# Kernel optimization log

Hardware: AMD Instinct MI355X
Metric: run time of the kernel (lower is better)

## Reference

```python
import jax, jax.numpy as jnp
import numpy as np

WS = 8                       # window size (square)
N = WS * WS                  # tokens per window
RES_H, RES_W = 32, 32        # input_resolution
DIM = 512
NUM_HEADS = 16
HEAD_DIM = DIM // NUM_HEADS
SCALE = HEAD_DIM ** -0.5
TABLE = 2 * WS - 1           # size of a_p/b_p/a_r/b_r tables
B_ = 1024                    # num_windows * batch


def _rel_coords():
    c = np.arange(WS)
    coords = np.stack(np.meshgrid(c, c, indexing='ij'))          # (2, WS, WS)
    cf = coords.reshape(2, -1)                                   # (2, N)
    rel = cf[:, :, None] - cf[:, None, :]                        # (2, N, N), values in [-(WS-1), WS-1]
    return rel[0], rel[1]                                        # radius (dh), azimuth (dw)

RADIUS_NP, AZIMUTH_NP = _rel_coords()
# torch indexes the (2*WS-1)-row tables with negative indices -> python wrap: -k maps to TABLE-k
IDX_R = jnp.asarray(RADIUS_NP % TABLE)
IDX_AZ = jnp.asarray(AZIMUTH_NP % TABLE)
RADIUS = jnp.asarray(RADIUS_NP, dtype=jnp.float32)               # (N, N)
AZIMUTH = jnp.asarray(AZIMUTH_NP, dtype=jnp.float32)             # (N, N)


def setup_inputs() -> dict:
    key = jax.random.key(0)
    ks = jax.random.split(key, 10)
    return {
        'x': jax.random.normal(ks[0], (B_, N, DIM), dtype=jnp.float32),
        'theta_max': jnp.ones((), dtype=jnp.float32) * 1.5708,   # ~pi/2 field-of-view half-angle
        'qkv_w': jax.random.normal(ks[1], (3 * DIM, DIM), dtype=jnp.float32) * 0.02,
        'qkv_b': jnp.zeros((3 * DIM,), dtype=jnp.float32),
        'proj_w': jax.random.normal(ks[2], (DIM, DIM), dtype=jnp.float32) * 0.02,
        'proj_b': jnp.zeros((DIM,), dtype=jnp.float32),
        'a_p': jax.random.normal(ks[3], (TABLE, NUM_HEADS), dtype=jnp.float32) * 0.02,
        'b_p': jax.random.normal(ks[4], (TABLE, NUM_HEADS), dtype=jnp.float32) * 0.02,
        'a_r': jax.random.normal(ks[5], (TABLE, NUM_HEADS), dtype=jnp.float32) * 0.02,
        'b_r': jax.random.normal(ks[6], (TABLE, NUM_HEADS), dtype=jnp.float32) * 0.02,
    }


def _trig_bias(table_a, table_b, idx, angle):
    # table_[ab]: (TABLE, H); idx: (N, N) int; angle: (N, N) float (possibly traced)
    a = table_a[idx]                                              # (N, N, H)
    b = table_b[idx]
    ang = angle[:, :, None]                                       # (N, N, 1)
    bias = a * jnp.cos(ang) + b * jnp.sin(ang)                    # (N, N, H)
    return jnp.transpose(bias, (2, 0, 1))                         # (H, N, N)


def reference(x, theta_max, qkv_w, qkv_b, proj_w, proj_b, a_p, b_p, a_r, b_r):
    Bw, n, c = x.shape
    qkv = x @ qkv_w.T + qkv_b                                     # (B_, N, 3*DIM)
    qkv = qkv.reshape(Bw, n, 3, NUM_HEADS, HEAD_DIM)
    qkv = jnp.transpose(qkv, (2, 0, 3, 1, 4))                     # (3, B_, H, N, hd)
    q, k, v = qkv[0] * SCALE, qkv[1], qkv[2]

    attn = jnp.einsum('bhid,bhjd->bhij', q, k)                    # (B_, H, N, N)

    az_angle = AZIMUTH * (2.0 * np.pi / RES_W)                    # (N, N)
    A_phi = _trig_bias(a_p, b_p, IDX_AZ, az_angle)                # (H, N, N)
    r_angle = RADIUS * (theta_max / RES_H)                        # (N, N), traced via theta_max
    A_theta = _trig_bias(a_r, b_r, IDX_R, r_angle)                # (H, N, N)

    attn = attn + A_phi[None] + A_theta[None]
    attn = jax.nn.softmax(attn, axis=-1)

    out = jnp.einsum('bhij,bhjd->bhid', attn, v)                  # (B_, H, N, hd)
    out = jnp.transpose(out, (0, 2, 1, 3)).reshape(Bw, n, c)      # (B_, N, DIM)
    out = out @ proj_w.T + proj_b
    return out
```

## Files before the change

kernel.cpp:

```cpp
#include <hip/hip_runtime.h>
#include <hip/hip_bf16.h>


typedef __bf16 bf16_t;
typedef bf16_t bf16x4 __attribute__((ext_vector_type(4)));
typedef bf16_t bf16x8 __attribute__((ext_vector_type(8)));
typedef float  f32x4  __attribute__((ext_vector_type(4)));

#define NWIN   1024
#define NTOK   64
#define DIM    512
#define NHEADS 16
#define HD     32
#define MTOT   (NWIN*NTOK)
#define QKVN   (3*DIM)
#define SCLG2E 0.25503494f

__device__ __forceinline__ void async_copy16(const void* g, void* lds_generic) {
    __builtin_amdgcn_global_load_lds(
        (__attribute__((address_space(1))) unsigned int*)(unsigned long long)g,
        (__attribute__((address_space(3))) unsigned int*)(unsigned int)(unsigned long long)lds_generic,
        16, 0, 0);
}

__global__ void cvt_f32_bf16(const float* __restrict__ in, bf16_t* __restrict__ out, int n8) {
    int i = blockIdx.x * blockDim.x + threadIdx.x;
    if (i >= n8) return;
    const float4* p = (const float4*)in;
    float4 a = p[2*i], b = p[2*i+1];
    bf16x8 o;
    o[0]=(bf16_t)a.x; o[1]=(bf16_t)a.y; o[2]=(bf16_t)a.z; o[3]=(bf16_t)a.w;
    o[4]=(bf16_t)b.x; o[5]=(bf16_t)b.y; o[6]=(bf16_t)b.z; o[7]=(bf16_t)b.w;
    ((bf16x8*)out)[i] = o;
}

__global__ void bias_kernel(const float* __restrict__ ap, const float* __restrict__ bp,
                            const float* __restrict__ ar, const float* __restrict__ br,
                            const float* __restrict__ theta_max, float* __restrict__ bias) {
    int idx = blockIdx.x * 256 + threadIdx.x;
    int h  = idx >> 12;
    int ij = idx & 4095;
    int i = ij >> 6, j = ij & 63;
    int ri = i >> 3, ci = i & 7, rj = j >> 3, cj = j & 7;
    int rad = ri - rj, az = ci - cj;
    int idx_r  = rad < 0 ? rad + 15 : rad;
    int idx_az = az  < 0 ? az  + 15 : az;
    float azang = (float)az * 0.19634954084936207f;
    float rang  = (float)rad * (theta_max[0] * (1.0f/32.0f));
    float v = ap[idx_az*NHEADS + h] * cosf(azang) + bp[idx_az*NHEADS + h] * sinf(azang)
            + ar[idx_r *NHEADS + h] * cosf(rang)  + br[idx_r *NHEADS + h] * sinf(rang);
    bias[idx] = v * 1.4426950408889634f;
}

template<int OUT_BF16>
__global__ __launch_bounds__(512, 2)
void gemm_bt(const bf16_t* __restrict__ A, const bf16_t* __restrict__ Bt,
             const float* __restrict__ bias, void* __restrict__ C,
             int M, int N, int K, int ntiles) {
    __shared__ bf16_t sA[3][256*64];
    __shared__ bf16_t sB[3][128*64];

    int nwg = gridDim.x;
    int bid = blockIdx.x;
    int wg = ((nwg & 7) == 0) ? ((bid & 7) * (nwg >> 3) + (bid >> 3)) : bid;
    int bm = wg / ntiles, bn = wg % ntiles;

    int tid = threadIdx.x;
    int w = tid >> 6, lane = tid & 63;
    int quad = lane >> 4, l16 = lane & 15;
    int wm = w >> 2, wn = w & 3;

    const bf16_t* Abase = A  + (size_t)(bm*256) * K;
    const bf16_t* Bbase = Bt + (size_t)(bn*128) * K;

    int T = K >> 6;

    auto STAGE = [&](int t) {
        int q = t - (t/3)*3;
        int k0 = t << 6;
        #pragma unroll
        for (int i = 0; i < 4; ++i) {
            int off = (i*512 + tid) << 4;
            int r  = off >> 7;
            int pb = (off >> 4) & 7;
            int cb = pb ^ (r & 7);
            async_copy16(Abase + (size_t)r*K + k0 + cb*8,
                         (char*)sA[q] + i*8192 + w*1024);
        }
        #pragma unroll
        for (int i = 0; i < 2; ++i) {
            int off = (i*512 + tid) << 4;
            int r  = off >> 7;
            int pb = (off >> 4) & 7;
            int cb = pb ^ (r & 7);
            async_copy16(Bbase + (size_t)r*K + k0 + cb*8,
                         (char*)sB[q] + i*8192 + w*1024);
        }
    };

    f32x4 acc[8][2] = {};

    STAGE(0);
    if (T > 1) STAGE(1);

    #pragma unroll 1
    for (int t = 0; t < T; ++t) {
        if (t < T - 1) asm volatile("s_waitcnt vmcnt(6)" ::: "memory");
        else           asm volatile("s_waitcnt vmcnt(0)" ::: "memory");
        __builtin_amdgcn_s_barrier();
        if (t + 2 < T) STAGE(t + 2);

        int q = t - (t/3)*3;
        const char* cA = (const char*)sA[q];
        const char* cB = (const char*)sB[q];
        #pragma unroll
        for (int kk = 0; kk < 64; kk += 32) {
            bf16x8 af[8], bfr[2];
            #pragma unroll
            for (int mi = 0; mi < 8; ++mi) {
                int r  = wm*128 + mi*16 + l16;
                int cb = (kk >> 3) + quad;
                int pb = cb ^ (r & 7);
                af[mi] = *(const bf16x8*)(cA + r*128 + pb*16);
            }
            #pragma unroll
            for (int ni = 0; ni < 2; ++ni) {
                int r  = wn*32 + ni*16 + l16;
                int cb = (kk >> 3) + quad;
                int pb = cb ^ (r & 7);
                bfr[ni] = *(const bf16x8*)(cB + r*128 + pb*16);
            }
            #pragma unroll
            for (int mi = 0; mi < 8; ++mi)
                #pragma unroll
                for (int ni = 0; ni < 2; ++ni)
                    acc[mi][ni] = __builtin_amdgcn_mfma_f32_16x16x32_bf16(
                        af[mi], bfr[ni], acc[mi][ni], 0, 0, 0);
        }
    }

    #pragma unroll
    for (int ni = 0; ni < 2; ++ni) {
        int col = bn*128 + wn*32 + ni*16 + l16;
        float bv = bias[col];
        #pragma unroll
        for (int mi = 0; mi < 8; ++mi) {
            int row0 = bm*256 + wm*128 + mi*16 + quad*4;
            f32x4 a = acc[mi][ni];
            #pragma unroll
            for (int reg = 0; reg < 4; ++reg) {
                float v = a[reg] + bv;
                size_t o = (size_t)(row0 + reg) * N + col;
                if (OUT_BF16) ((bf16_t*)C)[o] = (bf16_t)v;
                else          ((float*)C)[o]  = v;
            }
        }
    }
}

__global__ __launch_bounds__(256, 4)
void attn_kernel(const bf16_t* __restrict__ qkv, const float* __restrict__ bias,
                 bf16_t* __restrict__ obuf) {
    __shared__ bf16_t pbuf[4][2048];

    int b = blockIdx.x;
    int tid = threadIdx.x;
    int w = tid >> 6, lane = tid & 63, quad = lane >> 4, l16 = lane & 15;
    int qh = quad >> 1, ql = quad & 1;
    const bf16_t* base = qkv + (size_t)(b*64) * QKVN;
    f32x4 zero = {0.f, 0.f, 0.f, 0.f};
    bf16_t* pb = pbuf[w];

    #pragma unroll 1
    for (int t = 0; t < 4; ++t) {
        int h = w*4 + t;

        bf16x8 ak[4], bq[4];
        #pragma unroll
        for (int jt = 0; jt < 4; ++jt)
            ak[jt] = *(const bf16x8*)(base + (size_t)(jt*16 + l16)*QKVN + 512 + h*32 + quad*8);
        #pragma unroll
        for (int it = 0; it < 4; ++it)
            bq[it] = *(const bf16x8*)(base + (size_t)(it*16 + l16)*QKVN + h*32 + quad*8);

        bf16x8 av[2][2];
        #pragma unroll
        for (int dt = 0; dt < 2; ++dt)
            #pragma unroll
            for (int ks = 0; ks < 2; ++ks) {
                const bf16_t* vb = base + (size_t)(ks*32 + quad*8)*QKVN + 1024 + h*32 + dt*16 + l16;
                bf16x8 tmp;
                #pragma unroll
                for (int e = 0; e < 8; ++e) tmp[e] = vb[(size_t)e*QKVN];
                av[dt][ks] = tmp;
            }

        const float* bh = bias + h*4096;
        f32x4 accO[2][4];
        float s[4];
        #pragma unroll
        for (int it = 0; it < 4; ++it) { s[it] = 0.f; accO[0][it] = zero; accO[1][it] = zero; }

        #pragma unroll
        for (int ks = 0; ks < 2; ++ks) {
            f32x4 bb[2][4];
            #pragma unroll
            for (int jh = 0; jh < 2; ++jh)
                #pragma unroll
                for (int it = 0; it < 4; ++it)
                    bb[jh][it] = *(const f32x4*)(bh + (it*16 + l16)*64 + (ks*2+jh)*16 + quad*4);

            f32x4 st[2][4];
            #pragma unroll
            for (int jh = 0; jh < 2; ++jh)
                #pragma unroll
                for (int it = 0; it < 4; ++it)
                    st[jh][it] = __builtin_amdgcn_mfma_f32_16x16x32_bf16(ak[ks*2+jh], bq[it], zero, 0, 0, 0);

            #pragma unroll
            for (int it = 0; it < 4; ++it)
                #pragma unroll
                for (int jh = 0; jh < 2; ++jh) {
                    float e0 = __builtin_amdgcn_exp2f(st[jh][it][0]*SCLG2E + bb[jh][it][0]);
                    float e1 = __builtin_amdgcn_exp2f(st[jh][it][1]*SCLG2E + bb[jh][it][1]);
                    float e2 = __builtin_amdgcn_exp2f(st[jh][it][2]*SCLG2E + bb[jh][it][2]);
                    float e3 = __builtin_amdgcn_exp2f(st[jh][it][3]*SCLG2E + bb[jh][it][3]);
                    s[it] += (e0 + e1) + (e2 + e3);
                    bf16x4 pk4;
                    pk4[0] = (bf16_t)e0; pk4[1] = (bf16_t)e1;
                    pk4[2] = (bf16_t)e2; pk4[3] = (bf16_t)e3;
                    *(bf16x4*)(pb + it*512 + (2*jh + qh)*128 + l16*8 + ql*4) = pk4;
                }

            #pragma unroll
            for (int it = 0; it < 4; ++it) {
                bf16x8 bp = ((const bf16x8*)(pb + it*512))[lane];
                accO[0][it] = __builtin_amdgcn_mfma_f32_16x16x32_bf16(av[0][ks], bp, accO[0][it], 0, 0, 0);
                accO[1][it] = __builtin_amdgcn_mfma_f32_16x16x32_bf16(av[1][ks], bp, accO[1][it], 0, 0, 0);
            }
        }

        #pragma unroll
        for (int it = 0; it < 4; ++it) {
            float sv = s[it];
            sv += __shfl_xor(sv, 16);
            sv += __shfl_xor(sv, 32);
            float inv = __builtin_amdgcn_rcpf(sv);
            #pragma unroll
            for (int dt = 0; dt < 2; ++dt) {
                bf16x4 o4;
                #pragma unroll
                for (int r = 0; r < 4; ++r) o4[r] = (bf16_t)(accO[dt][it][r] * inv);
                *(bf16x4*)(obuf + (size_t)(b*64 + it*16 + l16)*DIM + h*32 + dt*16 + quad*4) = o4;
            }
        }
    }
}

extern "C" void kernel_launch(void* const* d_in, const int* in_sizes, int n_in,
                              void* d_out, int out_size, void* d_ws, size_t ws_size,
                              hipStream_t stream) {
    const float* x      = (const float*)d_in[0];
    const float* theta  = (const float*)d_in[1];
    const float* qkv_w  = (const float*)d_in[2];
    const float* qkv_b  = (const float*)d_in[3];
    const float* proj_w = (const float*)d_in[4];
    const float* proj_b = (const float*)d_in[5];
    const float* a_p    = (const float*)d_in[6];
    const float* b_p    = (const float*)d_in[7];
    const float* a_r    = (const float*)d_in[8];
    const float* b_r    = (const float*)d_in[9];
    float* out = (float*)d_out;

    char* ws = (char*)d_ws;
    bf16_t* qkvbuf = (bf16_t*)ws;
    bf16_t* xb     = (bf16_t*)(ws + 201326592);
    bf16_t* wqkv   = (bf16_t*)(ws + 201326592 + 67108864);
    bf16_t* wproj  = (bf16_t*)(ws + 201326592 + 67108864 + 1572864);
    float*  biasbf = (float*) (ws + 201326592 + 67108864 + 1572864 + 524288);
    bf16_t* obuf   = xb;

    cvt_f32_bf16<<<(MTOT*DIM/8)/256, 256, 0, stream>>>(x, xb, MTOT*DIM/8);
    cvt_f32_bf16<<<(QKVN*DIM/8)/256, 256, 0, stream>>>(qkv_w, wqkv, QKVN*DIM/8);
    cvt_f32_bf16<<<(DIM*DIM/8)/256, 256, 0, stream>>>(proj_w, wproj, DIM*DIM/8);

    bias_kernel<<<256, 256, 0, stream>>>(a_p, b_p, a_r, b_r, theta, biasbf);

    gemm_bt<1><<<(MTOT/256)*(QKVN/128), 512, 0, stream>>>(xb, wqkv, qkv_b, qkvbuf,
                                                          MTOT, QKVN, DIM, QKVN/128);
    attn_kernel<<<NWIN, 256, 0, stream>>>(qkvbuf, biasbf, obuf);

    gemm_bt<0><<<(MTOT/256)*(DIM/128), 512, 0, stream>>>(obuf, wproj, proj_b, out,
                                                         MTOT, DIM, DIM, DIM/128);
}
```

Baseline: 561.6 us.

## Rework GEMM to 256x256 tiles with half-K ping-pong LDS pipeline

The bf16 GEMM used for the QKV and output projections now computes 256x256 output tiles instead of 256x128. It double-buffers LDS in 32-wide K halves with a new XOR swizzle. Async global-to-LDS loads are interleaved with MFMA phases separated by barriers and raised wave priority, in the style of a ping-pong schedule. This is meant to raise arithmetic intensity per tile and hide load latency. In exchange it doubles the accumulator registers, halves the grid size, which lowers occupancy and tail balance, and adds many barriers.

New measurement: 679.7 us. +21.0%, slower.

```diff
diff --git a/kernel.cpp b/kernel.cpp
--- a/kernel.cpp
+++ b/kernel.cpp
@@ -15,6 +15,8 @@
 #define MTOT   (NWIN*NTOK)
 #define QKVN   (3*DIM)
 #define SCLG2E 0.25503494f
+
+#define BAR()  do { __builtin_amdgcn_s_barrier(); asm volatile("" ::: "memory"); } while (0)
 
 __device__ __forceinline__ void async_copy16(const void* g, void* lds_generic) {
     __builtin_amdgcn_global_load_lds(
@@ -57,8 +59,7 @@
 void gemm_bt(const bf16_t* __restrict__ A, const bf16_t* __restrict__ Bt,
              const float* __restrict__ bias, void* __restrict__ C,
              int M, int N, int K, int ntiles) {
-    __shared__ bf16_t sA[3][256*64];
-    __shared__ bf16_t sB[3][128*64];
+    __shared__ bf16_t lds[2][2][2][8192];
 
     int nwg = gridDim.x;
     int bid = blockIdx.x;
@@ -71,77 +72,99 @@
     int wm = w >> 2, wn = w & 3;
 
     const bf16_t* Abase = A  + (size_t)(bm*256) * K;
-    const bf16_t* Bbase = Bt + (size_t)(bn*128) * K;
+    const bf16_t* Bbase = Bt + (size_t)(bn*256) * K;
 
     int T = K >> 6;
-
-    auto STAGE = [&](int t) {
-        int q = t - (t/3)*3;
-        int k0 = t << 6;
-        #pragma unroll
-        for (int i = 0; i < 4; ++i) {
-            int off = (i*512 + tid) << 4;
-            int r  = off >> 7;
-            int pb = (off >> 4) & 7;
-            int cb = pb ^ (r & 7);
-            async_copy16(Abase + (size_t)r*K + k0 + cb*8,
-                         (char*)sA[q] + i*8192 + w*1024);
-        }
-        #pragma unroll
-        for (int i = 0; i < 2; ++i) {
-            int off = (i*512 + tid) << 4;
-            int r  = off >> 7;
-            int pb = (off >> 4) & 7;
-            int cb = pb ^ (r & 7);
-            async_copy16(Bbase + (size_t)r*K + k0 + cb*8,
-                         (char*)sB[q] + i*8192 + w*1024);
+    int niter = T >> 1;
+
+    auto STAGE = [&](const bf16_t* Mb, int mat, int t, int h) {
+        int q = t & 1;
+        int k0 = (t << 6) + (h << 5);
+        char* dst = (char*)&lds[q][mat][h][0] + w*1024;
+        #pragma unroll
+        for (int j = 0; j < 2; ++j) {
+            int slot = j*512 + tid;
+            int r  = slot >> 2;
+            int cb = (slot & 3) ^ ((r >> 1) & 3);
+            async_copy16(Mb + (size_t)r*K + k0 + cb*8, dst + j*8192);
         }
     };
 
-    f32x4 acc[8][2] = {};
-
-    STAGE(0);
-    if (T > 1) STAGE(1);
+    auto LDA = [&](int q, int h, bf16x8* af) {
+        const char* b_ = (const char*)&lds[q][0][h][0];
+        #pragma unroll
+        for (int mi = 0; mi < 8; ++mi) {
+            int r = wm*128 + mi*16 + l16;
+            af[mi] = *(const bf16x8*)(b_ + r*64 + ((quad ^ ((r >> 1) & 3)) << 4));
+        }
+    };
+    auto LDB = [&](int q, int h, int n0, bf16x8* bf2) {
+        const char* b_ = (const char*)&lds[q][1][h][0];
+        #pragma unroll
+        for (int k = 0; k < 2; ++k) {
+            int r = wn*64 + (n0 + k)*16 + l16;
+            bf2[k] = *(const bf16x8*)(b_ + r*64 + ((quad ^ ((r >> 1) & 3)) << 4));
+        }
+    };
+
+    f32x4 acc[8][4] = {};
+
+    auto MMA = [&](bf16x8* af, bf16x8* bf2, int n0) {
+        __builtin_amdgcn_s_setprio(1);
+        #pragma unroll
+        for (int mi = 0; mi < 8; ++mi)
+            #pragma unroll
+            for (int k = 0; k < 2; ++k)
+                acc[mi][n0 + k] = __builtin_amdgcn_mfma_f32_16x16x32_bf16(
+                    af[mi], bf2[k], acc[mi][n0 + k], 0, 0, 0);
+        __builtin_amdgcn_s_setprio(0);
+    };
+
+    STAGE(Abase, 0, 0, 0); STAGE(Bbase, 1, 0, 0);
+    STAGE(Abase, 0, 0, 1); STAGE(Bbase, 1, 0, 1);
+    STAGE(Abase, 0, 1, 0); STAGE(Bbase, 1, 1, 0);
+    asm volatile("s_waitcnt vmcnt(4)" ::: "memory");
+    BAR();
 
     #pragma unroll 1
-    for (int t = 0; t < T; ++t) {
-        if (t < T - 1) asm volatile("s_waitcnt vmcnt(6)" ::: "memory");
-        else           asm volatile("s_waitcnt vmcnt(0)" ::: "memory");
-        __builtin_amdgcn_s_barrier();
-        if (t + 2 < T) STAGE(t + 2);
-
-        int q = t - (t/3)*3;
-        const char* cA = (const char*)sA[q];
-        const char* cB = (const char*)sB[q];
-        #pragma unroll
-        for (int kk = 0; kk < 64; kk += 32) {
-            bf16x8 af[8], bfr[2];
-            #pragma unroll
-            for (int mi = 0; mi < 8; ++mi) {
-                int r  = wm*128 + mi*16 + l16;
-                int cb = (kk >> 3) + quad;
-                int pb = cb ^ (r & 7);
-                af[mi] = *(const bf16x8*)(cA + r*128 + pb*16);
-            }
-            #pragma unroll
-            for (int ni = 0; ni < 2; ++ni) {
-                int r  = wn*32 + ni*16 + l16;
-                int cb = (kk >> 3) + quad;
-                int pb = cb ^ (r & 7);
-                bfr[ni] = *(const bf16x8*)(cB + r*128 + pb*16);
-            }
-            #pragma unroll
-            for (int mi = 0; mi < 8; ++mi)
-                #pragma unroll
-                for (int ni = 0; ni < 2; ++ni)
-                    acc[mi][ni] = __builtin_amdgcn_mfma_f32_16x16x32_bf16(
-                        af[mi], bfr[ni], acc[mi][ni], 0, 0, 0);
-        }
+    for (int i = 0; i < niter; ++i) {
+        int t0 = 2*i, t1 = 2*i + 1;
+        bool last = (i == niter - 1);
+        bf16x8 af[8], bf2[2];
+
+        LDA(0, 0, af); LDB(0, 0, 0, bf2);
+        STAGE(Abase, 0, t1, 1);
+        BAR(); MMA(af, bf2, 0); BAR();
+        LDB(0, 0, 2, bf2);
+        STAGE(Bbase, 1, t1, 1);
+        BAR(); MMA(af, bf2, 2); BAR();
+        LDA(0, 1, af); LDB(0, 1, 0, bf2);
+        if (t0 + 2 < T) STAGE(Abase, 0, t0 + 2, 0);
+        BAR(); MMA(af, bf2, 0); BAR();
+        LDB(0, 1, 2, bf2);
+        if (t0 + 2 < T) STAGE(Bbase, 1, t0 + 2, 0);
+        if (last) asm volatile("s_waitcnt vmcnt(0)" ::: "memory");
+        else      asm volatile("s_waitcnt vmcnt(4)" ::: "memory");
+        BAR(); MMA(af, bf2, 2); BAR();
+        LDA(1, 0, af); LDB(1, 0, 0, bf2);
+        if (t0 + 2 < T) STAGE(Abase, 0, t0 + 2, 1);
+        BAR(); MMA(af, bf2, 0); BAR();
+        LDB(1, 0, 2, bf2);
+        if (t0 + 2 < T) STAGE(Bbase, 1, t0 + 2, 1);
+        BAR(); MMA(af, bf2, 2); BAR();
+        LDA(1, 1, af); LDB(1, 1, 0, bf2);
+        if (t1 + 2 < T) STAGE(Abase, 0, t1 + 2, 0);
+        BAR(); MMA(af, bf2, 0); BAR();
+        LDB(1, 1, 2, bf2);
+        if (t1 + 2 < T) STAGE(Bbase, 1, t1 + 2, 0);
+        if (last) asm volatile("s_waitcnt vmcnt(0)" ::: "memory");
+        else      asm volatile("s_waitcnt vmcnt(4)" ::: "memory");
+        BAR(); MMA(af, bf2, 2); BAR();
     }
 
     #pragma unroll
-    for (int ni = 0; ni < 2; ++ni) {
-        int col = bn*128 + wn*32 + ni*16 + l16;
+    for (int ni = 0; ni < 4; ++ni) {
+        int col = bn*256 + wn*64 + ni*16 + l16;
         float bv = bias[col];
         #pragma unroll
         for (int mi = 0; mi < 8; ++mi) {
@@ -286,10 +309,10 @@
 
     bias_kernel<<<256, 256, 0, stream>>>(a_p, b_p, a_r, b_r, theta, biasbf);
 
-    gemm_bt<1><<<(MTOT/256)*(QKVN/128), 512, 0, stream>>>(xb, wqkv, qkv_b, qkvbuf,
-                                                          MTOT, QKVN, DIM, QKVN/128);
+    gemm_bt<1><<<(MTOT/256)*(QKVN/256), 512, 0, stream>>>(xb, wqkv, qkv_b, qkvbuf,
+                                                          MTOT, QKVN, DIM, QKVN/256);
     attn_kernel<<<NWIN, 256, 0, stream>>>(qkvbuf, biasbf, obuf);
 
-    gemm_bt<0><<<(MTOT/256)*(DIM/128), 512, 0, stream>>>(obuf, wproj, proj_b, out,
-                                                         MTOT, DIM, DIM, DIM/128);
-}
+    gemm_bt<0><<<(MTOT/256)*(DIM/256), 512, 0, stream>>>(obuf, wproj, proj_b, out,
+                                                         MTOT, DIM, DIM, DIM/256);
+}
```
